# Optimization experiments

Hardware: AMD Instinct MI355X
Metric: run time of the kernel (lower is better)

The kernel has to match this reference:

```python
import jax, jax.numpy as jnp
import numpy as np

GDEP = 2      # gcn_depth
ALPHA = 0.05  # propalpha


def _mixprop(x, adj, W, b):
    # x: [B, C, N, L], adj: [N, N], W: [C_out, (GDEP+1)*C], b: [C_out]
    N = adj.shape[0]
    adj = adj + jnp.eye(N, dtype=adj.dtype)
    a = adj / adj.sum(1)[:, None]          # row-normalized adjacency
    h = x
    outs = [h]
    for _ in range(GDEP):
        # h = alpha*x + (1-alpha) * A h  (hop diffusion with residual blend)
        h = ALPHA * x + (1.0 - ALPHA) * jnp.einsum('ncwl,vw->ncvl', h, a)
        outs.append(h)
    ho = jnp.concatenate(outs, axis=1)     # [B, (GDEP+1)*C, N, L]
    # 1x1 Conv2d == channel-mixing einsum
    return jnp.einsum('ncwl,oc->nowl', ho, W) + b[None, :, None, None]


def setup_inputs() -> dict:
    key = jax.random.key(0)
    k0, k1, k2, k3 = jax.random.split(key, 4)
    B, C, CR, N, L = 32, 32, 32, 160, 160  # L must equal N (see a_new = s @ a @ s)
    fan = (GDEP + 1) * C
    x = jax.random.normal(k0, (B, C, N, L), dtype=jnp.float32)
    a = jax.random.uniform(k1, (N, N), dtype=jnp.float32)
    We = jax.random.normal(k2, (C, fan), dtype=jnp.float32) / np.float32(np.sqrt(fan))
    be = jnp.zeros((C,), dtype=jnp.float32)
    Wp = jax.random.normal(k3, (CR, fan), dtype=jnp.float32) / np.float32(np.sqrt(fan))
    bp = jnp.zeros((CR,), dtype=jnp.float32)
    return {"x": x, "a": a, "We": We, "be": be, "Wp": Wp, "bp": bp}


def reference(x, a, We, be, Wp, bp):
    # embed1 / pool1 applied to a and a^T, summed
    embed = _mixprop(x, a, We, be) + _mixprop(x, a.T, We, be)   # [B, C, N, L]
    pool = _mixprop(x, a, Wp, bp) + _mixprop(x, a.T, Wp, bp)    # [B, CR, N, L]
    s = jax.nn.softmax(pool, axis=2)                            # softmax over node dim
    # x_new = s^T z : [B, CR, L, N] @ [B, C, N, L] -> [B, C, L, L] (CR == C)
    x_new = jnp.matmul(jnp.swapaxes(s, -1, -2), embed)
    # a_new = s @ a @ s : ([N,L]@[N,N])@[N,L], requires L == N
    a_new = jnp.matmul(jnp.matmul(s, a), s)
    return (x_new, a_new)
```

## Files before the change

### kernel.cpp

```cpp
#include <hip/hip_runtime.h>

#define NN 160
#define MAT (NN*NN)
#define BCN 1024
#define BIG ((size_t)BCN * MAT)
#define PKSZ 12800
#define ALPHA 0.05f
#define BETA  0.95f

typedef unsigned int u32;
typedef __attribute__((ext_vector_type(8))) short short8;
typedef __attribute__((ext_vector_type(4))) float f32x4;

static __device__ __forceinline__ u32 pk2(float lo, float hi) {
    u32 a = __float_as_uint(lo), b = __float_as_uint(hi);
    a += 0x7fffu + ((a >> 16) & 1u);
    b += 0x7fffu + ((b >> 16) & 1u);
    return (a >> 16) | (b & 0xffff0000u);
}

__global__ __launch_bounds__(256) void prep_sums(const float* __restrict__ a,
                                                 float* __restrict__ sums)
{
    __shared__ float rbuf[256], cbuf[256];
    int b = blockIdx.x, t = threadIdx.x;
    float r = 0.f, c = 0.f;
    if (t < NN) { r = a[b*NN + t]; c = a[t*NN + b]; }
    rbuf[t] = r; cbuf[t] = c;
    __syncthreads();
    for (int s = 128; s > 0; s >>= 1) {
        if (t < s) { rbuf[t] += rbuf[t+s]; cbuf[t] += cbuf[t+s]; }
        __syncthreads();
    }
    if (t == 0) {
        sums[b]      = 1.f / (rbuf[0] + 1.f);
        sums[NN + b] = 1.f / (cbuf[0] + 1.f);
    }
}

__global__ __launch_bounds__(256) void prep_norm(
    const float* __restrict__ a, const float* __restrict__ sums,
    float* __restrict__ A1f, float* __restrict__ A2f)
{
    int i = blockIdx.x * 256 + threadIdx.x;
    int v = i / NN, w = i % NN;
    float d = (v == w) ? 1.f : 0.f;
    A1f[i] = (a[v*NN + w] + d) * sums[v];
    A2f[i] = (a[w*NN + v] + d) * sums[NN + v];
}

__global__ __launch_bounds__(256) void prep_mm(
    const float* __restrict__ A1f, const float* __restrict__ A2f,
    float* __restrict__ Ab1f, float* __restrict__ Ab2f)
{
    int idx = blockIdx.x * 256 + threadIdx.x;
    int mtx = idx / MAT;
    int i = idx % MAT;
    int v = i / NN, l = i % NN;
    const float* A = mtx ? A2f : A1f;
    float s = 0.f;
    for (int w = 0; w < NN; ++w) s = fmaf(A[v*NN + w], A[w*NN + l], s);
    float d = (v == l) ? ALPHA : 0.f;
    float o = d + ALPHA*BETA*A[i] + BETA*BETA*s;
    (mtx ? Ab2f : Ab1f)[i] = o;
}

__global__ __launch_bounds__(256) void prep_pk(
    const float* __restrict__ a, const float* __restrict__ A1f,
    const float* __restrict__ A2f, const float* __restrict__ Ab1f,
    const float* __restrict__ Ab2f,
    u32* __restrict__ At12pk, u32* __restrict__ Ah12pk, u32* __restrict__ apk)
{
    int idx = blockIdx.x * 256 + threadIdx.x;
    if (idx >= 3 * 3200) return;
    int mtx = idx / 3200;
    int r = idx % 3200;
    int k8 = r / 160, v = r % 160;
    u32 o[4];
    #pragma unroll
    for (int j = 0; j < 4; ++j) {
        int w0 = k8*8 + 2*j;
        float f0, f1;
        if (mtx == 0) {
            f0 = BETA*(A1f[v*NN + w0]     + A2f[v*NN + w0])     + ((v == w0)   ? 2.f*ALPHA : 0.f);
            f1 = BETA*(A1f[v*NN + w0 + 1] + A2f[v*NN + w0 + 1]) + ((v == w0+1) ? 2.f*ALPHA : 0.f);
        } else if (mtx == 1) {
            f0 = Ab1f[v*NN + w0]     + Ab2f[v*NN + w0];
            f1 = Ab1f[v*NN + w0 + 1] + Ab2f[v*NN + w0 + 1];
        } else {
            f0 = a[v*NN + w0];
            f1 = a[v*NN + w0 + 1];
        }
        o[j] = pk2(f0, f1);
    }
    u32* dst = (mtx == 0) ? At12pk : (mtx == 1) ? Ah12pk : apk;
    *(uint4*)&dst[(k8*160 + v)*4] = make_uint4(o[0], o[1], o[2], o[3]);
}

__global__ __launch_bounds__(256) void prep_wpk(
    const float* __restrict__ We, const float* __restrict__ Wp,
    u32* __restrict__ Wpk)
{
    int idx = blockIdx.x * 256 + threadIdx.x;
    if (idx >= 768) return;
    int k8c = idx / 64, m = idx % 64;
    const float* W = (m < 32) ? We + m*96 : Wp + (m-32)*96;
    float sc = (k8c < 4) ? 2.f : 1.f;
    u32 o[4];
    #pragma unroll
    for (int j = 0; j < 4; ++j) {
        int c0 = k8c*8 + 2*j;
        o[j] = pk2(W[c0]*sc, W[c0+1]*sc);
    }
    *(uint4*)&Wpk[idx*4] = make_uint4(o[0], o[1], o[2], o[3]);
}

__global__ __launch_bounds__(256) void cvt_x_pk(const float* __restrict__ x,
                                                u32* __restrict__ xpk)
{
    int idx = blockIdx.x * 256 + threadIdx.x;
    int l  = idx % NN;
    int k8 = (idx / NN) % 20;
    int bc = idx / 3200;
    const float* xb = x + (size_t)bc * MAT + (size_t)(k8*8) * NN + l;
    u32 o[4];
    #pragma unroll
    for (int j = 0; j < 4; ++j)
        o[j] = pk2(xb[(2*j)*NN], xb[(2*j+1)*NN]);
    *(uint4*)&xpk[(size_t)bc * PKSZ + (size_t)(k8*160 + l)*4] =
        make_uint4(o[0], o[1], o[2], o[3]);
}

__global__ __launch_bounds__(256, 2) void bgemm16(
    const u32* __restrict__ Apk, long astride,
    const u32* __restrict__ Qpk,
    float* __restrict__ Cf, int cacc,
    u32* __restrict__ Cpk)
{
    __shared__ u32 As[2560];
    __shared__ u32 Bs[2560];
    int bc = blockIdx.x;
    int t = threadIdx.x;
    int lane = t & 63, w = t >> 6;
    int q = lane >> 4, ll = lane & 15;
    int v0w = (w >> 1) * 80, l0w = (w & 1) * 80;
    const u32* Ab = Apk + (size_t)bc * (size_t)astride;
    const u32* Qb = Qpk + (size_t)bc * PKSZ;

    f32x4 acc[5][5];
    #pragma unroll
    for (int rt = 0; rt < 5; ++rt)
        #pragma unroll
        for (int ct = 0; ct < 5; ++ct)
            acc[rt][ct] = (f32x4){0.f, 0.f, 0.f, 0.f};

    for (int c = 0; c < 5; ++c) {
        __syncthreads();
        for (int i = t; i < 640; i += 256) {
            *(uint4*)&As[i*4] = *(const uint4*)&Ab[(size_t)c*2560 + i*4];
            *(uint4*)&Bs[i*4] = *(const uint4*)&Qb[(size_t)c*2560 + i*4];
        }
        __syncthreads();
        short8 af[5], bf[5];
        #pragma unroll
        for (int rt = 0; rt < 5; ++rt)
            af[rt] = *(const short8*)&As[(q*160 + v0w + rt*16 + ll)*4];
        #pragma unroll
        for (int ct = 0; ct < 5; ++ct)
            bf[ct] = *(const short8*)&Bs[(q*160 + l0w + ct*16 + ll)*4];
        #pragma unroll
        for (int rt = 0; rt < 5; ++rt)
            #pragma unroll
            for (int ct = 0; ct < 5; ++ct)
                acc[rt][ct] = __builtin_amdgcn_mfma_f32_16x16x32_bf16(
                    af[rt], bf[ct], acc[rt][ct], 0, 0, 0);
    }

    float* Cb = Cf  ? Cf  + (size_t)bc * MAT  : (float*)0;
    u32*   Pb = Cpk ? Cpk + (size_t)bc * PKSZ : (u32*)0;
    #pragma unroll
    for (int rt = 0; rt < 5; ++rt) {
        int vb = v0w + rt*16 + q*4;
        #pragma unroll
        for (int ct = 0; ct < 5; ++ct) {
            int l = l0w + ct*16 + ll;
            f32x4 o = acc[rt][ct];
            if (Pb) {
                int k8 = vb >> 3, j = (vb >> 1) & 3;
                size_t pa = (size_t)(k8*160 + l)*4 + j;
                Pb[pa]     = pk2(o.x, o.y);
                Pb[pa + 1] = pk2(o.z, o.w);
            }
            if (Cb) {
                size_t base = (size_t)vb * NN + l;
                if (cacc) {
                    o.x += Cb[base];
                    o.y += Cb[base + NN];
                    o.z += Cb[base + 2*NN];
                    o.w += Cb[base + 3*NN];
                }
                Cb[base]        = o.x;
                Cb[base + NN]   = o.y;
                Cb[base + 2*NN] = o.z;
                Cb[base + 3*NN] = o.w;
            }
        }
    }
}

__global__ __launch_bounds__(256, 2) void chanmix_mm(
    const float* __restrict__ x, const float* __restrict__ g1,
    const float* __restrict__ g2, const u32* __restrict__ Wpk,
    const float* __restrict__ be, const float* __restrict__ bp,
    u32* __restrict__ embed_pk, float* __restrict__ pool)
{
    __shared__ u32 hs[12288];
    __shared__ u32 wl[3072];
    int t = threadIdx.x;
    int bid = blockIdx.x;
    int b   = bid / 100;
    int r   = bid % 100;
    int k8v = r / 5;
    int l0  = (r % 5) * 32;

    #pragma unroll
    for (int i = 0; i < 3; ++i) {
        int ii = i*256 + t;
        *(uint4*)&wl[ii*4] = *(const uint4*)&Wpk[ii*4];
    }

    {
        int vsub = t >> 5, lsub = t & 31;
        size_t poff  = (size_t)(k8v*8 + vsub) * NN + l0 + lsub;
        size_t bbase = (size_t)b * (size_t)(32*MAT);
        #pragma unroll 4
        for (int k8c = 0; k8c < 12; ++k8c) {
            u32 o4[4];
            #pragma unroll
            for (int j = 0; j < 4; ++j) {
                int c0 = k8c*8 + 2*j;
                const float* pl = (c0 < 32) ? x  + bbase + (size_t)c0*MAT
                                : (c0 < 64) ? g1 + bbase + (size_t)(c0-32)*MAT
                                            : g2 + bbase + (size_t)(c0-64)*MAT;
                o4[j] = pk2(pl[poff], pl[poff + MAT]);
            }
            *(uint4*)&hs[(k8c*256 + t)*4] = make_uint4(o4[0], o4[1], o4[2], o4[3]);
        }
    }
    __syncthreads();

    int lane = t & 63, w = t >> 6;
    int q = lane >> 4, ll = lane & 15;

    f32x4 acc[16];
    #pragma unroll
    for (int nt = 0; nt < 16; ++nt) acc[nt] = (f32x4){0.f, 0.f, 0.f, 0.f};

    #pragma unroll
    for (int kc = 0; kc < 3; ++kc) {
        short8 af = *(const short8*)&wl[((kc*4 + q)*64 + w*16 + ll)*4];
        #pragma unroll
        for (int nt = 0; nt < 16; ++nt) {
            short8 bf = *(const short8*)&hs[((kc*4 + q)*256 + nt*16 + ll)*4];
            acc[nt] = __builtin_amdgcn_mfma_f32_16x16x32_bf16(af, bf, acc[nt], 0, 0, 0);
        }
    }

    int m0 = w*16 + q*4;
    if (w >= 2) {
        #pragma unroll
        for (int nt = 0; nt < 16; ++nt) {
            int v = k8v*8 + (nt >> 1);
            int l = l0 + (nt & 1)*16 + ll;
            #pragma unroll
            for (int rg = 0; rg < 4; ++rg) {
                int o = m0 - 32 + rg;
                pool[(size_t)(b*32 + o)*MAT + (size_t)v*NN + l]
                    = acc[nt][rg] + 2.f*bp[o];
            }
        }
    } else {
        #pragma unroll
        for (int lh = 0; lh < 2; ++lh) {
            int l = l0 + lh*16 + ll;
            #pragma unroll
            for (int rg = 0; rg < 4; ++rg) {
                int o = m0 + rg;
                float bias = 2.f * be[o];
                uint4 u;
                u.x = pk2(acc[0  + lh][rg] + bias, acc[2  + lh][rg] + bias);
                u.y = pk2(acc[4  + lh][rg] + bias, acc[6  + lh][rg] + bias);
                u.z = pk2(acc[8  + lh][rg] + bias, acc[10 + lh][rg] + bias);
                u.w = pk2(acc[12 + lh][rg] + bias, acc[14 + lh][rg] + bias);
                *(uint4*)&embed_pk[(size_t)(b*32 + o)*PKSZ
                                   + (size_t)(k8v*160 + l)*4] = u;
            }
        }
    }
}

__global__ __launch_bounds__(256) void softmax_n(const float* __restrict__ p,
                                                 u32* __restrict__ srpk,
                                                 u32* __restrict__ scpk)
{
    int idx = blockIdx.x * 256 + threadIdx.x;
    int l  = idx % NN;
    int bo = idx / NN;
    const float* col = p + (size_t)bo * MAT + l;
    float m = -1e30f, s = 0.f;
    for (int n = 0; n < NN; ++n) {
        float v  = col[(size_t)n * NN];
        float mn = fmaxf(m, v);
        s = s * __expf(m - mn) + __expf(v - mn);
        m = mn;
    }
    float inv = 1.f / s;
    u32* sp = srpk + (size_t)bo * PKSZ;
    u32* cp = scpk + (size_t)bo * PKSZ;
    int k8c = l >> 3, jc = (l >> 1) & 3;
    bool wlane = ((l & 1) == 0);
    for (int k2 = 0; k2 < 80; ++k2) {
        float s0 = __expf(col[(size_t)(2*k2)   * NN] - m) * inv;
        float s1 = __expf(col[(size_t)(2*k2+1) * NN] - m) * inv;
        sp[(size_t)((k2 >> 2)*160 + l)*4 + (k2 & 3)] = pk2(s0, s1);
        float t0 = __shfl_down(s0, 1);
        float t1 = __shfl_down(s1, 1);
        if (wlane) {
            cp[(size_t)(k8c*160 + 2*k2)*4 + jc]     = pk2(s0, t0);
            cp[(size_t)(k8c*160 + 2*k2 + 1)*4 + jc] = pk2(s1, t1);
        }
    }
}

extern "C" void kernel_launch(void* const* d_in, const int* in_sizes, int n_in,
                              void* d_out, int out_size, void* d_ws, size_t ws_size,
                              hipStream_t stream)
{
    const float* x  = (const float*)d_in[0];
    const float* a  = (const float*)d_in[1];
    const float* We = (const float*)d_in[2];
    const float* be = (const float*)d_in[3];
    const float* Wp = (const float*)d_in[4];
    const float* bp = (const float*)d_in[5];

    float* part0 = (float*)d_out;
    float* part1 = part0 + BIG;

    char* ws = (char*)d_ws;
    u32* At12pk = (u32*)(ws + 0);
    u32* Ah12pk = (u32*)(ws + 51200);
    u32* apk    = (u32*)(ws + 102400);
    u32* Wpk    = (u32*)(ws + 153600);
    float* B1      = (float*)(ws + 256000);
    u32*   R3      = (u32*)  (ws + 256000 + 104857600);
    u32*   R4      = (u32*)  (ws + 256000 + 157286400);
    float* sums = B1;
    float* A1f  = (float*)((char*)B1 + 1536);
    float* A2f  = A1f + MAT;
    float* Ab1f = A2f + MAT;
    float* Ab2f = Ab1f + MAT;
    u32* x_pk     = R3;
    u32* embed_pk = R3;
    u32* srpk = (u32*)B1;
    u32* scpk = (u32*)((char*)B1 + 52428800);
    u32* M_pk = R4;

    prep_sums<<<160, 256, 0, stream>>>(a, sums);
    prep_norm<<<100, 256, 0, stream>>>(a, sums, A1f, A2f);
    prep_mm  <<<200, 256, 0, stream>>>(A1f, A2f, Ab1f, Ab2f);
    prep_pk  <<<38, 256, 0, stream>>>(a, A1f, A2f, Ab1f, Ab2f,
                                      At12pk, Ah12pk, apk);
    prep_wpk <<<3, 256, 0, stream>>>(We, Wp, Wpk);
    cvt_x_pk <<<12800, 256, 0, stream>>>(x, x_pk);

    bgemm16<<<BCN, 256, 0, stream>>>(At12pk, 0, x_pk, B1,    0, (u32*)0);
    bgemm16<<<BCN, 256, 0, stream>>>(Ah12pk, 0, x_pk, part1, 0, (u32*)0);

    chanmix_mm<<<3200, 256, 0, stream>>>(x, B1, part1, Wpk, be, bp,
                                         embed_pk, part0);
    softmax_n<<<640, 256, 0, stream>>>(part0, srpk, scpk);

    bgemm16<<<BCN, 256, 0, stream>>>(apk, 0, srpk, (float*)0, 0, M_pk);
    bgemm16<<<BCN, 256, 0, stream>>>(srpk, (long)PKSZ, embed_pk, part0, 0, (u32*)0);
    bgemm16<<<BCN, 256, 0, stream>>>(scpk, (long)PKSZ, M_pk, part1, 0, (u32*)0);
}
```

Baseline: 673.1 us.

## Merge paired batched GEMM launches and split softmax columns across four lanes

The batched bf16 MFMA GEMM body moves into a shared device function. The two hop-diffusion GEMMs become one 2048-block launch, with blocks interleaved so both adjacency variants read the same x tile close in time; it also raises launch bounds to 3 blocks per SM. The two output GEMMs are likewise merged into one launch. Softmax now splits each column across four threads and combines their partial max and sum with xor shuffles, giving four times the parallelism. The channel-mix kernel reads weights straight from global memory instead of staging them in LDS, trading an LDS copy and its footprint for uncached-in-LDS global reads.

```diff
diff --git a/kernel.cpp b/kernel.cpp
--- a/kernel.cpp
+++ b/kernel.cpp
@@ -131,21 +131,14 @@
         make_uint4(o[0], o[1], o[2], o[3]);
 }
 
-__global__ __launch_bounds__(256, 2) void bgemm16(
-    const u32* __restrict__ Apk, long astride,
-    const u32* __restrict__ Qpk,
-    float* __restrict__ Cf, int cacc,
-    u32* __restrict__ Cpk)
-{
-    __shared__ u32 As[2560];
-    __shared__ u32 Bs[2560];
-    int bc = blockIdx.x;
+static __device__ __forceinline__ void bgemm_core(
+    const u32* __restrict__ Ab, const u32* __restrict__ Qb,
+    float* Cb, int cacc, u32* Pb, u32* As, u32* Bs)
+{
     int t = threadIdx.x;
     int lane = t & 63, w = t >> 6;
     int q = lane >> 4, ll = lane & 15;
     int v0w = (w >> 1) * 80, l0w = (w & 1) * 80;
-    const u32* Ab = Apk + (size_t)bc * (size_t)astride;
-    const u32* Qb = Qpk + (size_t)bc * PKSZ;
 
     f32x4 acc[5][5];
     #pragma unroll
@@ -176,8 +169,6 @@
                     af[rt], bf[ct], acc[rt][ct], 0, 0, 0);
     }
 
-    float* Cb = Cf  ? Cf  + (size_t)bc * MAT  : (float*)0;
-    u32*   Pb = Cpk ? Cpk + (size_t)bc * PKSZ : (u32*)0;
     #pragma unroll
     for (int rt = 0; rt < 5; ++rt) {
         int vb = v0w + rt*16 + q*4;
@@ -208,6 +199,45 @@
     }
 }
 
+__global__ __launch_bounds__(256, 2) void bgemm16(
+    const u32* __restrict__ Apk, long astride,
+    const u32* __restrict__ Qpk,
+    float* __restrict__ Cf, int cacc,
+    u32* __restrict__ Cpk)
+{
+    __shared__ u32 As[2560], Bs[2560];
+    int bc = blockIdx.x;
+    bgemm_core(Apk + (size_t)bc * (size_t)astride,
+               Qpk + (size_t)bc * PKSZ,
+               Cf  ? Cf  + (size_t)bc * MAT  : (float*)0, cacc,
+               Cpk ? Cpk + (size_t)bc * PKSZ : (u32*)0, As, Bs);
+}
+
+__global__ __launch_bounds__(256, 3) void bgemm_hop(
+    const u32* __restrict__ A0, const u32* __restrict__ A1,
+    const u32* __restrict__ Q, float* __restrict__ C0, float* __restrict__ C1)
+{
+    __shared__ u32 As[2560], Bs[2560];
+    int bid = blockIdx.x;
+    int bc = ((bid >> 4) << 3) | (bid & 7);
+    int which = (bid >> 3) & 1;
+    bgemm_core(which ? A1 : A0,
+               Q + (size_t)bc * PKSZ,
+               (which ? C1 : C0) + (size_t)bc * MAT, 0, (u32*)0, As, Bs);
+}
+
+__global__ __launch_bounds__(256, 2) void bgemm_out(
+    const u32* __restrict__ Aa, const u32* __restrict__ Qa, float* __restrict__ Ca,
+    const u32* __restrict__ Ab2, const u32* __restrict__ Qb2, float* __restrict__ Cb2)
+{
+    __shared__ u32 As[2560], Bs[2560];
+    int which = blockIdx.x & 1;
+    int bc = blockIdx.x >> 1;
+    bgemm_core((which ? Ab2 : Aa) + (size_t)bc * PKSZ,
+               (which ? Qb2 : Qa) + (size_t)bc * PKSZ,
+               (which ? Cb2 : Ca) + (size_t)bc * MAT, 0, (u32*)0, As, Bs);
+}
+
 __global__ __launch_bounds__(256, 2) void chanmix_mm(
     const float* __restrict__ x, const float* __restrict__ g1,
     const float* __restrict__ g2, const u32* __restrict__ Wpk,
@@ -215,19 +245,12 @@
     u32* __restrict__ embed_pk, float* __restrict__ pool)
 {
     __shared__ u32 hs[12288];
-    __shared__ u32 wl[3072];
     int t = threadIdx.x;
     int bid = blockIdx.x;
     int b   = bid / 100;
     int r   = bid % 100;
     int k8v = r / 5;
     int l0  = (r % 5) * 32;
-
-    #pragma unroll
-    for (int i = 0; i < 3; ++i) {
-        int ii = i*256 + t;
-        *(uint4*)&wl[ii*4] = *(const uint4*)&Wpk[ii*4];
-    }
 
     {
         int vsub = t >> 5, lsub = t & 31;
@@ -258,7 +281,7 @@
 
     #pragma unroll
     for (int kc = 0; kc < 3; ++kc) {
-        short8 af = *(const short8*)&wl[((kc*4 + q)*64 + w*16 + ll)*4];
+        short8 af = *(const short8*)&Wpk[((kc*4 + q)*64 + w*16 + ll)*4];
         #pragma unroll
         for (int nt = 0; nt < 16; ++nt) {
             short8 bf = *(const short8*)&hs[((kc*4 + q)*256 + nt*16 + ll)*4];
@@ -304,14 +327,25 @@
                                                  u32* __restrict__ scpk)
 {
     int idx = blockIdx.x * 256 + threadIdx.x;
-    int l  = idx % NN;
-    int bo = idx / NN;
+    int h  = idx & 3;
+    int ci = idx >> 2;
+    int l  = ci % NN;
+    int bo = ci / NN;
     const float* col = p + (size_t)bo * MAT + l;
+    int n0 = h * 40;
     float m = -1e30f, s = 0.f;
-    for (int n = 0; n < NN; ++n) {
+    for (int n = n0; n < n0 + 40; ++n) {
         float v  = col[(size_t)n * NN];
         float mn = fmaxf(m, v);
         s = s * __expf(m - mn) + __expf(v - mn);
+        m = mn;
+    }
+    #pragma unroll
+    for (int d = 1; d <= 2; d <<= 1) {
+        float m2 = __shfl_xor(m, d);
+        float s2 = __shfl_xor(s, d);
+        float mn = fmaxf(m, m2);
+        s = s * __expf(m - mn) + s2 * __expf(m2 - mn);
         m = mn;
     }
     float inv = 1.f / s;
@@ -319,12 +353,12 @@
     u32* cp = scpk + (size_t)bo * PKSZ;
     int k8c = l >> 3, jc = (l >> 1) & 3;
     bool wlane = ((l & 1) == 0);
-    for (int k2 = 0; k2 < 80; ++k2) {
+    for (int k2 = h*20; k2 < h*20 + 20; ++k2) {
         float s0 = __expf(col[(size_t)(2*k2)   * NN] - m) * inv;
         float s1 = __expf(col[(size_t)(2*k2+1) * NN] - m) * inv;
         sp[(size_t)((k2 >> 2)*160 + l)*4 + (k2 & 3)] = pk2(s0, s1);
-        float t0 = __shfl_down(s0, 1);
-        float t1 = __shfl_down(s1, 1);
+        float t0 = __shfl_down(s0, 4);
+        float t1 = __shfl_down(s1, 4);
         if (wlane) {
             cp[(size_t)(k8c*160 + 2*k2)*4 + jc]     = pk2(s0, t0);
             cp[(size_t)(k8c*160 + 2*k2 + 1)*4 + jc] = pk2(s1, t1);
@@ -373,14 +407,13 @@
     prep_wpk <<<3, 256, 0, stream>>>(We, Wp, Wpk);
     cvt_x_pk <<<12800, 256, 0, stream>>>(x, x_pk);
 
-    bgemm16<<<BCN, 256, 0, stream>>>(At12pk, 0, x_pk, B1,    0, (u32*)0);
-    bgemm16<<<BCN, 256, 0, stream>>>(Ah12pk, 0, x_pk, part1, 0, (u32*)0);
+    bgemm_hop<<<2048, 256, 0, stream>>>(At12pk, Ah12pk, x_pk, B1, part1);
 
     chanmix_mm<<<3200, 256, 0, stream>>>(x, B1, part1, Wpk, be, bp,
                                          embed_pk, part0);
-    softmax_n<<<640, 256, 0, stream>>>(part0, srpk, scpk);
+    softmax_n<<<2560, 256, 0, stream>>>(part0, srpk, scpk);
 
     bgemm16<<<BCN, 256, 0, stream>>>(apk, 0, srpk, (float*)0, 0, M_pk);
-    bgemm16<<<BCN, 256, 0, stream>>>(srpk, (long)PKSZ, embed_pk, part0, 0, (u32*)0);
-    bgemm16<<<BCN, 256, 0, stream>>>(scpk, (long)PKSZ, M_pk, part1, 0, (u32*)0);
-}
+    bgemm_out<<<2048, 256, 0, stream>>>(srpk, embed_pk, part0,
+                                        scpk, M_pk, part1);
+}
```

New measurement: 674.9 us. No clear change (+0.3%).
